# Performance work log

Hardware: AMD Instinct MI355X
Metric: run time of the kernel (lower is better)

The kernel has to match this reference:

```python
import jax, jax.numpy as jnp
import numpy as np

D_MODEL = 512
N_HEAD = 8
D_HEAD = D_MODEL // N_HEAD


def setup_inputs() -> dict:
    key = jax.random.key(0)
    ks = jax.random.split(key, 8)
    B, S, T = 4, 512, 32
    src = jax.random.normal(ks[0], (B, S, D_MODEL), dtype=jnp.float32)
    tgt = jax.random.normal(ks[1], (B, S, T, D_MODEL), dtype=jnp.float32)
    tgt_padding_mask = jax.random.bernoulli(ks[2], 0.1, (B, S, T))
    scale = 1.0 / np.sqrt(D_MODEL)
    in_proj_weight = jax.random.uniform(ks[3], (3 * D_MODEL, D_MODEL), dtype=jnp.float32, minval=-scale, maxval=scale)
    in_proj_bias = jnp.zeros((3 * D_MODEL,), dtype=jnp.float32)
    out_proj_weight = jax.random.uniform(ks[4], (D_MODEL, D_MODEL), dtype=jnp.float32, minval=-scale, maxval=scale)
    out_proj_bias = jnp.zeros((D_MODEL,), dtype=jnp.float32)
    return {
        "src": src,
        "tgt": tgt,
        "tgt_padding_mask": tgt_padding_mask,
        "in_proj_weight": in_proj_weight,
        "in_proj_bias": in_proj_bias,
        "out_proj_weight": out_proj_weight,
        "out_proj_bias": out_proj_bias,
    }


def reference(src, tgt, tgt_padding_mask, in_proj_weight, in_proj_bias, out_proj_weight, out_proj_bias):
    # KNN-style cross attention branch (tgt is [B, S, T, D]).
    B, S, _ = src.shape
    T = tgt.shape[-2]
    w_src, w_tgt = in_proj_weight[:D_MODEL], in_proj_weight[D_MODEL:]
    b_src, b_tgt = in_proj_bias[:D_MODEL], in_proj_bias[D_MODEL:]

    q = src @ w_src.T + b_src                      # [B, S, D]
    kv = tgt @ w_tgt.T + b_tgt                     # [B, S, T, 2D]
    k, v = kv[..., :D_MODEL], kv[..., D_MODEL:]

    # mask handling: drop the mask for queries with no valid tgt, zero them later
    attn_invalid = tgt_padding_mask                # [B, S, T]
    mask_no_tgt_valid = jnp.all(attn_invalid, axis=-1)           # [B, S]
    attn_invalid = attn_invalid & ~mask_no_tgt_valid[..., None]

    q = q.reshape(B, S, N_HEAD, D_HEAD)            # [B, S, H, Dh]
    k = k.reshape(B, S, T, N_HEAD, D_HEAD)
    v = v.reshape(B, S, T, N_HEAD, D_HEAD)

    attn = jnp.einsum("bshd,bsthd->bhst", q, k)    # [B, H, S, T]
    attn = jnp.where(attn_invalid[:, None], -jnp.inf, attn)
    attn = jax.nn.softmax(attn / jnp.sqrt(jnp.asarray(D_HEAD, attn.dtype)), axis=-1)

    out = jnp.einsum("bhst,bsthd->bshd", attn, v).reshape(B, S, D_MODEL)
    out = out @ out_proj_weight.T + out_proj_bias
    out = jnp.where(mask_no_tgt_valid[..., None], 0.0, out)
    return out
```

## Files before the change

kernel.cpp:

```cpp
#include <hip/hip_runtime.h>
#include <hip/hip_bf16.h>

#define BS_   2048
#define T_    32
#define DM_   512
#define LDT   520

typedef __attribute__((ext_vector_type(8))) short frag8;
typedef __attribute__((ext_vector_type(4))) float f32x4;

__device__ __forceinline__ short f2s(float v) {
    return __builtin_bit_cast(short, __float2bfloat16(v));
}
__device__ __forceinline__ float s2f(short x) {
    return __builtin_bit_cast(float, (unsigned)(unsigned short)x << 16);
}
__device__ __forceinline__ void stv(float* p, float v)          { *p = v; }
__device__ __forceinline__ void stv(__hip_bfloat16* p, float v) { *p = __float2bfloat16(v); }

__device__ __forceinline__ void gl_lds16(const __hip_bfloat16* g, __hip_bfloat16* l) {
    __builtin_amdgcn_global_load_lds(
        (const __attribute__((address_space(1))) unsigned int*)g,
        (__attribute__((address_space(3))) unsigned int*)l, 16, 0, 0);
}

__global__ void cvt4(const float4* __restrict__ in, ushort4* __restrict__ out, int n4)
{
    int i = blockIdx.x * blockDim.x + threadIdx.x;
    if (i < n4) {
        float4 v = in[i];
        ushort4 o;
        o.x = (unsigned short)f2s(v.x); o.y = (unsigned short)f2s(v.y);
        o.z = (unsigned short)f2s(v.z); o.w = (unsigned short)f2s(v.w);
        out[i] = o;
    }
}

__global__ void tr_kv(const __hip_bfloat16* __restrict__ src,
                      __hip_bfloat16* __restrict__ dst)
{
    __shared__ __hip_bfloat16 tile[64][65];
    int bx = blockIdx.x, by = blockIdx.y;
    int tid = threadIdx.x;
#pragma unroll
    for (int i = 0; i < 16; ++i) {
        int idx = i * 256 + tid;
        int r = idx >> 6, c = idx & 63;
        tile[r][c] = src[(size_t)(bx * 64 + r) * 512 + by * 64 + c];
    }
    __syncthreads();
#pragma unroll
    for (int i = 0; i < 16; ++i) {
        int idx = i * 256 + tid;
        int rr = idx >> 6, cc = idx & 63;
        dst[(size_t)(by * 64 + rr) * 1024 + bx * 64 + cc] = tile[cc][rr];
    }
}

template<typename OUTT>
__global__ __launch_bounds__(256)
void gemm128(const __hip_bfloat16* __restrict__ A,
             const __hip_bfloat16* __restrict__ W,
             const float* __restrict__ bias,
             OUTT* __restrict__ C,
             const int* __restrict__ zrow,
             int M, int N, int K)
{
    __shared__ __hip_bfloat16 sA[128 * 64];
    __shared__ __hip_bfloat16 sB[128 * 64];

    int tid  = threadIdx.x;
    int lane = tid & 63;
    int wave = tid >> 6;
    int tn = blockIdx.x, tm = blockIdx.y;
    int wm = wave >> 1, wn = wave & 1;

    const __hip_bfloat16* Ab = A + (size_t)tm * 128 * K;
    const __hip_bfloat16* Wb = W + (size_t)tn * 128 * K;

    f32x4 acc[4][4];
#pragma unroll
    for (int i = 0; i < 4; ++i)
#pragma unroll
        for (int j = 0; j < 4; ++j) acc[i][j] = {0.f, 0.f, 0.f, 0.f};

    int wbase = (tid & ~63) * 8;
    int m  = lane & 15;
    int kq = (lane >> 4) * 8;

    for (int k0 = 0; k0 < K; k0 += 64) {
#pragma unroll
        for (int i = 0; i < 4; ++i) {
            int u = i * 256 + tid;
            gl_lds16(Ab + (size_t)(u >> 3) * K + k0 + (u & 7) * 8, &sA[i * 2048 + wbase]);
        }
#pragma unroll
        for (int i = 0; i < 4; ++i) {
            int u = i * 256 + tid;
            gl_lds16(Wb + (size_t)(u >> 3) * K + k0 + (u & 7) * 8, &sB[i * 2048 + wbase]);
        }
        __syncthreads();
#pragma unroll
        for (int ki = 0; ki < 2; ++ki) {
            frag8 af[4], bf[4];
#pragma unroll
            for (int i = 0; i < 4; ++i)
                af[i] = *(const frag8*)&sA[(wm * 64 + i * 16 + m) * 64 + ki * 32 + kq];
#pragma unroll
            for (int j = 0; j < 4; ++j)
                bf[j] = *(const frag8*)&sB[(wn * 64 + j * 16 + m) * 64 + ki * 32 + kq];
#pragma unroll
            for (int i = 0; i < 4; ++i)
#pragma unroll
                for (int j = 0; j < 4; ++j)
                    acc[i][j] = __builtin_amdgcn_mfma_f32_16x16x32_bf16(
                        af[i], bf[j], acc[i][j], 0, 0, 0);
        }
        __syncthreads();
    }

    int rb = (lane >> 4) * 4;
#pragma unroll
    for (int j = 0; j < 4; ++j) {
        int   col = tn * 128 + wn * 64 + j * 16 + m;
        float bv  = bias[col];
#pragma unroll
        for (int i = 0; i < 4; ++i) {
            int row0 = tm * 128 + wm * 64 + i * 16 + rb;
#pragma unroll
            for (int t = 0; t < 4; ++t) {
                int   row = row0 + t;
                float v   = acc[i][j][t] + bv;
                if (zrow && zrow[row]) v = 0.f;
                stv(&C[(size_t)row * N + col], v);
            }
        }
    }
}

__global__ __launch_bounds__(256)
void gemm_bt_g(const __hip_bfloat16* __restrict__ A, int lda, long astr,
               const __hip_bfloat16* __restrict__ W, int ldw, long wstr,
               const float* __restrict__ bias, int bstr,
               __hip_bfloat16* __restrict__ C, int ldc, long cstr,
               int M, int N, int K)
{
    int z = blockIdx.y;
    A += (size_t)z * astr;  W += (size_t)z * wstr;  C += (size_t)z * cstr;
    int bcol0 = z * bstr;

    int wave = blockIdx.x * 4 + (threadIdx.x >> 6);
    int lane = threadIdx.x & 63;
    int ntn  = N / 32;
    int tm = wave / ntn, tn = wave - tm * ntn;
    if (tm * 32 >= M) return;

    int r  = lane & 15;
    int kq = (lane >> 4) << 3;
    const __hip_bfloat16* Ap = A + (size_t)(tm * 32 + r) * lda + kq;
    const __hip_bfloat16* Wp = W + (size_t)(tn * 32 + r) * ldw + kq;

    f32x4 acc[2][2];
#pragma unroll
    for (int i = 0; i < 2; ++i)
#pragma unroll
        for (int j = 0; j < 2; ++j) acc[i][j] = {0.f, 0.f, 0.f, 0.f};

    for (int k0 = 0; k0 < K; k0 += 32) {
        frag8 a[2], b[2];
#pragma unroll
        for (int i = 0; i < 2; ++i) a[i] = *(const frag8*)(Ap + (size_t)i * 16 * lda + k0);
#pragma unroll
        for (int j = 0; j < 2; ++j) b[j] = *(const frag8*)(Wp + (size_t)j * 16 * ldw + k0);
#pragma unroll
        for (int i = 0; i < 2; ++i)
#pragma unroll
            for (int j = 0; j < 2; ++j)
                acc[i][j] = __builtin_amdgcn_mfma_f32_16x16x32_bf16(a[i], b[j], acc[i][j], 0, 0, 0);
    }

    int rb = (lane >> 4) * 4;
#pragma unroll
    for (int j = 0; j < 2; ++j) {
        int   col = tn * 32 + j * 16 + r;
        float bv  = bias ? bias[bcol0 + col] : 0.f;
#pragma unroll
        for (int i = 0; i < 2; ++i) {
            int row0 = tm * 32 + i * 16 + rb;
#pragma unroll
            for (int t = 0; t < 4; ++t)
                C[(size_t)(row0 + t) * ldc + col] =
                    __float2bfloat16(acc[i][j][t] + bv);
        }
    }
}

__global__ __launch_bounds__(256)
void fused_attn(const float* __restrict__ tgt,
                const __hip_bfloat16* __restrict__ qkh,
                const int* __restrict__ mask,
                __hip_bfloat16* __restrict__ tbar,
                int* __restrict__ zrow)
{
    int bs  = blockIdx.x;
    int tid = threadIdx.x;

    __shared__ __hip_bfloat16 sT[32 * LDT];
    __shared__ __hip_bfloat16 sQK[4096];
    __shared__ float sP[8][32];
    __shared__ int   sM[32];

    const float* tg = tgt + (size_t)bs * 32 * 512;
#pragma unroll
    for (int i = 0; i < 16; ++i) {
        int idx = i * 256 + tid;
        int row = idx >> 7, c4 = (idx & 127) * 4;
        float4 v = *(const float4*)(tg + (size_t)row * 512 + c4);
        ushort4 o;
        o.x = (unsigned short)f2s(v.x); o.y = (unsigned short)f2s(v.y);
        o.z = (unsigned short)f2s(v.z); o.w = (unsigned short)f2s(v.w);
        *(ushort4*)&sT[row * LDT + c4] = o;
    }
    const ushort4* qk4 = (const ushort4*)(qkh + (size_t)bs * 4096);
#pragma unroll
    for (int i = 0; i < 4; ++i) {
        int idx = i * 256 + tid;
        ((ushort4*)sQK)[idx] = qk4[idx];
    }
    if (tid < 32) sM[tid] = mask[bs * 32 + tid];
    __syncthreads();

    bool allm = true;
#pragma unroll
    for (int t = 0; t < 32; ++t) allm = allm && (sM[t] != 0);

    int h = tid >> 5, t = tid & 31;
    const __hip_bfloat16* qrow = sQK + h * 512;
    const __hip_bfloat16* trow = &sT[t * LDT];
    float s = 0.f;
#pragma unroll
    for (int c8 = 0; c8 < 64; ++c8) {
        frag8 a = *(const frag8*)(trow + c8 * 8);
        frag8 b = *(const frag8*)(qrow + c8 * 8);
#pragma unroll
        for (int j = 0; j < 8; ++j) s += s2f(a[j]) * s2f(b[j]);
    }
    s *= 0.125f;
    if (!allm && sM[t]) s = -__builtin_inff();

    float mx = s;
    for (int off = 16; off; off >>= 1) mx = fmaxf(mx, __shfl_xor(mx, off, 32));
    float e = __expf(s - mx);
    float sum = e;
    for (int off = 16; off; off >>= 1) sum += __shfl_xor(sum, off, 32);
    sP[h][t] = e / sum;
    if (tid == 0) zrow[bs] = allm ? 1 : 0;
    __syncthreads();

    int h2 = tid >> 5, c0 = (tid & 31) * 16;
    float acc[16];
#pragma unroll
    for (int j = 0; j < 16; ++j) acc[j] = 0.f;
#pragma unroll
    for (int tt = 0; tt < 32; ++tt) {
        float p = sP[h2][tt];
        frag8 v1 = *(const frag8*)&sT[tt * LDT + c0];
        frag8 v2 = *(const frag8*)&sT[tt * LDT + c0 + 8];
#pragma unroll
        for (int j = 0; j < 8; ++j) { acc[j] += p * s2f(v1[j]); acc[8 + j] += p * s2f(v2[j]); }
    }
    ushort4 o1, o2, o3, o4;
    o1.x = (unsigned short)f2s(acc[0]);  o1.y = (unsigned short)f2s(acc[1]);
    o1.z = (unsigned short)f2s(acc[2]);  o1.w = (unsigned short)f2s(acc[3]);
    o2.x = (unsigned short)f2s(acc[4]);  o2.y = (unsigned short)f2s(acc[5]);
    o2.z = (unsigned short)f2s(acc[6]);  o2.w = (unsigned short)f2s(acc[7]);
    o3.x = (unsigned short)f2s(acc[8]);  o3.y = (unsigned short)f2s(acc[9]);
    o3.z = (unsigned short)f2s(acc[10]); o3.w = (unsigned short)f2s(acc[11]);
    o4.x = (unsigned short)f2s(acc[12]); o4.y = (unsigned short)f2s(acc[13]);
    o4.z = (unsigned short)f2s(acc[14]); o4.w = (unsigned short)f2s(acc[15]);
    ushort4* dst = (ushort4*)(tbar + (size_t)bs * 4096 + h2 * 512 + c0);
    dst[0] = o1; dst[1] = o2; dst[2] = o3; dst[3] = o4;
}

extern "C" void kernel_launch(void* const* d_in, const int* in_sizes, int n_in,
                              void* d_out, int out_size, void* d_ws, size_t ws_size,
                              hipStream_t stream)
{
    const float* src  = (const float*)d_in[0];
    const float* tgt  = (const float*)d_in[1];
    const int*   mask = (const int*)d_in[2];
    const float* ipw  = (const float*)d_in[3];
    const float* ipb  = (const float*)d_in[4];
    const float* opw  = (const float*)d_in[5];
    const float* opb  = (const float*)d_in[6];
    float*       out  = (float*)d_out;

    char* ws = (char*)d_ws;
    __hip_bfloat16* src_bf = (__hip_bfloat16*)(ws);
    __hip_bfloat16* ipw_bf = (__hip_bfloat16*)(ws + ((size_t)2 << 20));
    __hip_bfloat16* opw_bf = (__hip_bfloat16*)(ws + ((size_t)2 << 20) + 1536 * 512 * 2);
    __hip_bfloat16* q_bf   = (__hip_bfloat16*)(ws + ((size_t)4 << 20));
    __hip_bfloat16* Tk     = (__hip_bfloat16*)(ws + ((size_t)6 << 20));
    __hip_bfloat16* qkh    = (__hip_bfloat16*)(ws + ((size_t)8 << 20));
    __hip_bfloat16* tbar   = (__hip_bfloat16*)(ws + ((size_t)24 << 20));
    __hip_bfloat16* ao_bf  = (__hip_bfloat16*)(ws + ((size_t)40 << 20));
    int*            zrow   = (int*)(ws + ((size_t)42 << 20));

    cvt4<<<(1536 * 512 / 4) / 256, 256, 0, stream>>>((const float4*)ipw, (ushort4*)ipw_bf, 1536 * 512 / 4);
    cvt4<<<(512 * 512 / 4) / 256, 256, 0, stream>>>((const float4*)opw, (ushort4*)opw_bf, 512 * 512 / 4);
    cvt4<<<(2048 * 512 / 4) / 256, 256, 0, stream>>>((const float4*)src, (ushort4*)src_bf, 2048 * 512 / 4);

    tr_kv<<<dim3(16, 8), 256, 0, stream>>>(ipw_bf + (size_t)512 * 512, Tk);

    gemm128<__hip_bfloat16><<<dim3(4, 16), 256, 0, stream>>>(
        src_bf, ipw_bf, ipb, q_bf, nullptr, BS_, DM_, DM_);

    gemm_bt_g<<<dim3(256, 8), 256, 0, stream>>>(
        q_bf, 512, 64,  Tk, 1024, 64,  nullptr, 0,
        qkh, 4096, 512,  BS_, 512, 64);

    fused_attn<<<BS_, 256, 0, stream>>>(tgt, qkh, mask, tbar, zrow);

    gemm_bt_g<<<dim3(32, 8), 256, 0, stream>>>(
        tbar, 4096, 512,  ipw_bf + (size_t)1024 * 512, 512, (long)64 * 512,
        ipb + 1024, 64,
        ao_bf, 512, 64,  BS_, 64, 512);

    gemm128<float><<<dim3(4, 16), 256, 0, stream>>>(
        ao_bf, opw_bf, opb, out, zrow, BS_, DM_, DM_);
}
```

Baseline: 283.4 us.

## Fuse prep conversions into one kernel and swizzle LDS accesses to cut bank conflicts

Merges the three fp32-to-bf16 conversion launches and the K-weight transpose into a single prep kernel, which reads the fp32 weights directly for the transpose. This saves three launches and the dependent transpose pass. The GEMM now stores LDS tiles with an XOR swizzle on the k-chunk, and the attention kernel rotates its per-thread loop start, both to reduce LDS bank conflicts. In exchange the kernel carries more index arithmetic and a branchy prep kernel.

```diff
diff --git a/kernel.cpp b/kernel.cpp
--- a/kernel.cpp
+++ b/kernel.cpp
@@ -24,36 +24,43 @@
         (__attribute__((address_space(3))) unsigned int*)l, 16, 0, 0);
 }
 
-__global__ void cvt4(const float4* __restrict__ in, ushort4* __restrict__ out, int n4)
-{
-    int i = blockIdx.x * blockDim.x + threadIdx.x;
-    if (i < n4) {
-        float4 v = in[i];
+__global__ __launch_bounds__(256)
+void prep(const float* __restrict__ ipw, const float* __restrict__ opw,
+          const float* __restrict__ src,
+          __hip_bfloat16* __restrict__ ipw_bf, __hip_bfloat16* __restrict__ opw_bf,
+          __hip_bfloat16* __restrict__ src_bf, __hip_bfloat16* __restrict__ Tk)
+{
+    __shared__ __hip_bfloat16 tile[64][65];
+    int b = blockIdx.x;
+    if (b < 2048) {
+        int g = b * 256 + threadIdx.x;
+        const float4* in; ushort4* out; int off;
+        if (g < 196608)      { in = (const float4*)ipw; out = (ushort4*)ipw_bf; off = g; }
+        else if (g < 262144) { in = (const float4*)opw; out = (ushort4*)opw_bf; off = g - 196608; }
+        else                 { in = (const float4*)src; out = (ushort4*)src_bf; off = g - 262144; }
+        float4 v = in[off];
         ushort4 o;
         o.x = (unsigned short)f2s(v.x); o.y = (unsigned short)f2s(v.y);
         o.z = (unsigned short)f2s(v.z); o.w = (unsigned short)f2s(v.w);
-        out[i] = o;
-    }
-}
-
-__global__ void tr_kv(const __hip_bfloat16* __restrict__ src,
-                      __hip_bfloat16* __restrict__ dst)
-{
-    __shared__ __hip_bfloat16 tile[64][65];
-    int bx = blockIdx.x, by = blockIdx.y;
-    int tid = threadIdx.x;
-#pragma unroll
-    for (int i = 0; i < 16; ++i) {
-        int idx = i * 256 + tid;
-        int r = idx >> 6, c = idx & 63;
-        tile[r][c] = src[(size_t)(bx * 64 + r) * 512 + by * 64 + c];
-    }
-    __syncthreads();
-#pragma unroll
-    for (int i = 0; i < 16; ++i) {
-        int idx = i * 256 + tid;
-        int rr = idx >> 6, cc = idx & 63;
-        dst[(size_t)(by * 64 + rr) * 1024 + bx * 64 + cc] = tile[cc][rr];
+        out[off] = o;
+    } else {
+        int bb = b - 2048;
+        int bx = bb & 15, by = bb >> 4;
+        int tid = threadIdx.x;
+        const float* sp = ipw + (size_t)512 * 512;
+#pragma unroll
+        for (int i = 0; i < 16; ++i) {
+            int idx = i * 256 + tid;
+            int r = idx >> 6, c = idx & 63;
+            tile[r][c] = __float2bfloat16(sp[(size_t)(bx * 64 + r) * 512 + by * 64 + c]);
+        }
+        __syncthreads();
+#pragma unroll
+        for (int i = 0; i < 16; ++i) {
+            int idx = i * 256 + tid;
+            int rr = idx >> 6, cc = idx & 63;
+            Tk[(size_t)(by * 64 + rr) * 1024 + bx * 64 + cc] = tile[cc][rr];
+        }
     }
 }
 
@@ -86,29 +93,28 @@
 
     int wbase = (tid & ~63) * 8;
     int m  = lane & 15;
-    int kq = (lane >> 4) * 8;
+    int q  = lane >> 4;
+    int sw = (m & 7) * 8;
+    int trow = tid >> 3;
+    int tcb  = ((tid & 7) ^ (trow & 7)) * 8;
 
     for (int k0 = 0; k0 < K; k0 += 64) {
 #pragma unroll
-        for (int i = 0; i < 4; ++i) {
-            int u = i * 256 + tid;
-            gl_lds16(Ab + (size_t)(u >> 3) * K + k0 + (u & 7) * 8, &sA[i * 2048 + wbase]);
-        }
-#pragma unroll
-        for (int i = 0; i < 4; ++i) {
-            int u = i * 256 + tid;
-            gl_lds16(Wb + (size_t)(u >> 3) * K + k0 + (u & 7) * 8, &sB[i * 2048 + wbase]);
-        }
+        for (int i = 0; i < 4; ++i)
+            gl_lds16(Ab + (size_t)(i * 32 + trow) * K + k0 + tcb, &sA[i * 2048 + wbase]);
+#pragma unroll
+        for (int i = 0; i < 4; ++i)
+            gl_lds16(Wb + (size_t)(i * 32 + trow) * K + k0 + tcb, &sB[i * 2048 + wbase]);
         __syncthreads();
 #pragma unroll
         for (int ki = 0; ki < 2; ++ki) {
             frag8 af[4], bf[4];
 #pragma unroll
             for (int i = 0; i < 4; ++i)
-                af[i] = *(const frag8*)&sA[(wm * 64 + i * 16 + m) * 64 + ki * 32 + kq];
+                af[i] = *(const frag8*)&sA[(wm * 64 + i * 16 + m) * 64 + (((ki * 4 + q) * 8) ^ sw)];
 #pragma unroll
             for (int j = 0; j < 4; ++j)
-                bf[j] = *(const frag8*)&sB[(wn * 64 + j * 16 + m) * 64 + ki * 32 + kq];
+                bf[j] = *(const frag8*)&sB[(wn * 64 + j * 16 + m) * 64 + (((ki * 4 + q) * 8) ^ sw)];
 #pragma unroll
             for (int i = 0; i < 4; ++i)
 #pragma unroll
@@ -237,11 +243,13 @@
     int h = tid >> 5, t = tid & 31;
     const __hip_bfloat16* qrow = sQK + h * 512;
     const __hip_bfloat16* trow = &sT[t * LDT];
+    int rot = t >> 3;
     float s = 0.f;
 #pragma unroll
     for (int c8 = 0; c8 < 64; ++c8) {
-        frag8 a = *(const frag8*)(trow + c8 * 8);
-        frag8 b = *(const frag8*)(qrow + c8 * 8);
+        int c = (c8 + rot) & 63;
+        frag8 a = *(const frag8*)(trow + c * 8);
+        frag8 b = *(const frag8*)(qrow + c * 8);
 #pragma unroll
         for (int j = 0; j < 8; ++j) s += s2f(a[j]) * s2f(b[j]);
     }
@@ -257,15 +265,17 @@
     if (tid == 0) zrow[bs] = allm ? 1 : 0;
     __syncthreads();
 
-    int h2 = tid >> 5, c0 = (tid & 31) * 16;
+    int h2 = tid >> 5, j32 = tid & 31, c0 = j32 * 16;
+    int rot2 = j32 >> 2;
     float acc[16];
 #pragma unroll
     for (int j = 0; j < 16; ++j) acc[j] = 0.f;
 #pragma unroll
     for (int tt = 0; tt < 32; ++tt) {
-        float p = sP[h2][tt];
-        frag8 v1 = *(const frag8*)&sT[tt * LDT + c0];
-        frag8 v2 = *(const frag8*)&sT[tt * LDT + c0 + 8];
+        int tp = (tt + rot2) & 31;
+        float p = sP[h2][tp];
+        frag8 v1 = *(const frag8*)&sT[tp * LDT + c0];
+        frag8 v2 = *(const frag8*)&sT[tp * LDT + c0 + 8];
 #pragma unroll
         for (int j = 0; j < 8; ++j) { acc[j] += p * s2f(v1[j]); acc[8 + j] += p * s2f(v2[j]); }
     }
@@ -306,11 +316,7 @@
     __hip_bfloat16* ao_bf  = (__hip_bfloat16*)(ws + ((size_t)40 << 20));
     int*            zrow   = (int*)(ws + ((size_t)42 << 20));
 
-    cvt4<<<(1536 * 512 / 4) / 256, 256, 0, stream>>>((const float4*)ipw, (ushort4*)ipw_bf, 1536 * 512 / 4);
-    cvt4<<<(512 * 512 / 4) / 256, 256, 0, stream>>>((const float4*)opw, (ushort4*)opw_bf, 512 * 512 / 4);
-    cvt4<<<(2048 * 512 / 4) / 256, 256, 0, stream>>>((const float4*)src, (ushort4*)src_bf, 2048 * 512 / 4);
-
-    tr_kv<<<dim3(16, 8), 256, 0, stream>>>(ipw_bf + (size_t)512 * 512, Tk);
+    prep<<<2176, 256, 0, stream>>>(ipw, opw, src, ipw_bf, opw_bf, src_bf, Tk);
 
     gemm128<__hip_bfloat16><<<dim3(4, 16), 256, 0, stream>>>(
         src_bf, ipw_bf, ipb, q_bf, nullptr, BS_, DM_, DM_);
```

Result: no change. 278.5 us (-1.7%).
